# Kernel optimization log

Measured on AMD Instinct MI355X. Metric: run time of the kernel, lower is better.

## Reference

```python
import jax, jax.numpy as jnp
import numpy as np

NUM_NODES = 39   # nodes per graph (hardcoded in module)
K = 10           # kNN neighbors (hardcoded)
HID = 256
NUM_CLASSES = 2
B = 512          # number of graphs
EPS = 1e-5


def _edge_conv(xg, W, b):
    """DynamicEdgeConv with max aggregation.
    xg: [B, N, F]. Builds kNN graph per-graph (Euclidean), edge feature
    [x_i, x_j - x_i], MLP(ReLU), max over neighbors. Self is its own
    nearest neighbor (matches torch_cluster.knn with x==y).
    """
    bsz, n, f = xg.shape
    sq = jnp.sum(xg * xg, axis=-1)                      # [B, N]
    d = sq[:, :, None] + sq[:, None, :] - 2.0 * jnp.einsum('bnf,bmf->bnm', xg, xg)
    _, idx = jax.lax.top_k(-d, K)                       # [B, N, K] smallest distances
    xj = xg[jnp.arange(bsz)[:, None, None], idx]        # [B, N, K, F]
    xi = xg[:, :, None, :]                              # [B, N, 1, F]
    e = jnp.concatenate([jnp.broadcast_to(xi, xj.shape), xj - xi], axis=-1)  # [B,N,K,2F]
    h = jax.nn.relu(jnp.einsum('bnkc,ch->bnkh', e, W) + b)
    return jnp.max(h, axis=2)                           # [B, N, H]


def _bn(h, gamma, beta):
    # BatchNorm1d over all nodes (training-mode batch stats, biased var)
    mean = jnp.mean(h, axis=(0, 1), keepdims=True)
    var = jnp.var(h, axis=(0, 1), keepdims=True)
    return (h - mean) * jax.lax.rsqrt(var + EPS) * gamma + beta


def setup_inputs() -> dict:
    key = jax.random.key(0)
    ks = jax.random.split(key, 12)
    f_in = NUM_NODES
    x = jax.random.normal(ks[0], (B * NUM_NODES, f_in), dtype=jnp.float32)
    batch = jnp.repeat(jnp.arange(B, dtype=jnp.int32), NUM_NODES)
    def lin(k, fin, fout):
        s = 1.0 / np.sqrt(fin)
        k1, k2 = jax.random.split(k)
        W = jax.random.uniform(k1, (fin, fout), jnp.float32, -s, s)
        b = jax.random.uniform(k2, (fout,), jnp.float32, -s, s)
        return W, b
    W1, b1 = lin(ks[1], 2 * f_in, HID)
    W2, b2 = lin(ks[2], 2 * HID, HID)
    W3, b3 = lin(ks[3], 2 * HID, HID)
    Wl, bl = lin(ks[4], HID, NUM_CLASSES)
    g1 = jnp.ones((HID,), jnp.float32); be1 = jnp.zeros((HID,), jnp.float32)
    g2 = jnp.ones((HID,), jnp.float32); be2 = jnp.zeros((HID,), jnp.float32)
    g3 = jnp.ones((HID,), jnp.float32); be3 = jnp.zeros((HID,), jnp.float32)
    return dict(x=x, batch=batch, W1=W1, b1=b1, W2=W2, b2=b2, W3=W3, b3=b3,
                g1=g1, be1=be1, g2=g2, be2=be2, g3=g3, be3=be3, Wl=Wl, bl=bl)


def reference(x, batch, W1, b1, W2, b2, W3, b3, g1, be1, g2, be2, g3, be3, Wl, bl):
    # Graphs are contiguous with fixed NUM_NODES nodes each (batch == repeat(arange(B))),
    # so reshape implements per-graph kNN and global_mean_pool exactly.
    bsz = x.shape[0] // NUM_NODES
    xg = x.reshape(bsz, NUM_NODES, -1)
    h = _edge_conv(xg, W1, b1)
    h = jax.nn.relu(_bn(h, g1, be1))
    h = _edge_conv(h, W2, b2)
    h = jax.nn.relu(_bn(h, g2, be2))
    h = _edge_conv(h, W3, b3)
    h = _bn(h, g3, be3)
    pooled = jnp.mean(h, axis=1)                        # global_mean_pool -> [B, H]
    logits = pooled @ Wl + bl
    return jax.nn.softmax(logits, axis=1)
```

## Files before the change

### kernel.cpp

```cpp
#include <hip/hip_runtime.h>
#include <hip/hip_bf16.h>
#include <stdint.h>

#define NG 512
#define NN 39
#define FIN0 39
#define HID 256
#define KNN 10
#define NROWS (NG * NN)
#define BNEPS 1e-5f

typedef __hip_bfloat16 bf16;
typedef __attribute__((ext_vector_type(8))) short s16x8;
typedef __attribute__((ext_vector_type(4))) float f32x4;

__device__ __forceinline__ void split_bf16(float v, bf16& hi, bf16& lo) {
  hi = __float2bfloat16(v);
  lo = __float2bfloat16(v - __bfloat162float(hi));
}

__device__ __forceinline__ void ld_b128(s16x8& d, const bf16* base, unsigned voff) {
  asm volatile("global_load_dwordx4 %0, %1, %2" : "=v"(d) : "v"(voff), "s"(base));
}
__device__ __forceinline__ void ld_f32x4(f32x4& d, const float* base, unsigned voff) {
  asm volatile("global_load_dwordx4 %0, %1, %2" : "=v"(d) : "v"(voff), "s"(base));
}
#define WAITV4 do { asm volatile("s_waitcnt vmcnt(4)"); __builtin_amdgcn_sched_barrier(0); } while (0)
#define WAITV0 do { asm volatile("s_waitcnt vmcnt(0)"); __builtin_amdgcn_sched_barrier(0); } while (0)

__device__ __forceinline__ float wfold(const float* __restrict__ W, int F, int c, int k) {
  if (k >= F) return 0.f;
  return (c < HID) ? (W[k * HID + c] - W[(F + k) * HID + c])
                   : W[(F + k) * HID + (c - HID)];
}

__global__ void k_prepw(const float* __restrict__ W1, const float* __restrict__ W2,
                        const float* __restrict__ W3,
                        bf16* __restrict__ W1Th, bf16* __restrict__ W1Tl,
                        bf16* __restrict__ W2Th, bf16* __restrict__ W2Tl,
                        bf16* __restrict__ W3Th, bf16* __restrict__ W3Tl) {
  int d = (blockIdx.x * 256 + threadIdx.x) * 4;
  const float* W; bf16 *Th, *Tl; int nks, F;
  if (d < 512 * 64) { W = W1; Th = W1Th; Tl = W1Tl; nks = 2; F = FIN0; }
  else {
    d -= 512 * 64;
    if (d < 512 * 256) { W = W2; Th = W2Th; Tl = W2Tl; nks = 8; F = HID; }
    else {
      d -= 512 * 256;
      if (d < 512 * 256) { W = W3; Th = W3Th; Tl = W3Tl; nks = 8; F = HID; }
      else return;
    }
  }
  const int frag = d >> 9, wi = d & 511, li = wi >> 3, e0 = wi & 7;
  const int fr = li & 15, fq = li >> 4;
  const int ks = frag % nks, cb = frag / nks;
  const int c = (cb >> 2) * 64 + 4 * fr + (cb & 3);
  const int k0 = ks * 32 + fq * 8 + e0;
  union U { bf16 b[4]; uint64_t u; } h, l;
#pragma unroll
  for (int t = 0; t < 4; t++) split_bf16(wfold(W, F, c, k0 + t), h.b[t], l.b[t]);
  *(uint64_t*)(Th + d) = h.u;
  *(uint64_t*)(Tl + d) = l.u;
}

#define VSTR 260
#define RSTR 260
template <int K, bool FIRST>
__global__ __launch_bounds__(512, 4) void k_fused(const float* __restrict__ fin,
                                                  const float* __restrict__ st,
                                                  const bf16* __restrict__ BTh,
                                                  const bf16* __restrict__ BTl,
                                                  const float* __restrict__ bias,
                                                  float* __restrict__ h_out,
                                                  float* __restrict__ part) {
  constexpr int XBYTES = 48 * K * 2 * 2;
  constexpr int ALIAS = (NN * VSTR + 8 * RSTR) * 4;
  constexpr int SBASE = (XBYTES > ALIAS) ? XBYTES : ((ALIAS + 15) & ~15);
  __shared__ __align__(16) char smem[SBASE + 6240 + 160 + 1568];
  bf16* Xh = (bf16*)smem;
  bf16* Xl = Xh + 48 * K;
  float* vsh = (float*)smem;
  float* red = (float*)(smem + NN * VSTR * 4);
  float* dmat = (float*)(smem + SBASE);
  float* sqv  = (float*)(smem + SBASE + 6240);
  int*   idxs = (int*)(smem + SBASE + 6240 + 160);

  const int b = blockIdx.x, tid = threadIdx.x;
  const int wv = tid >> 6, ln = tid & 63;
  const int fr = ln & 15, fq = ln >> 4;
  const size_t base = (size_t)b * NN;
  constexpr int NKS = K / 32;

  if (FIRST) {
    if (tid < 48 * 8) {
      const int row = tid >> 3, g = tid & 7;
      union { bf16 b8[8]; s16x8 v; } ph, pl;
      if (row < NN) {
#pragma unroll
        for (int j = 0; j < 8; j++) {
          const int k = g * 8 + j;
          const float x = (k < FIN0) ? fin[(base + row) * FIN0 + k] : 0.f;
          split_bf16(x, ph.b8[j], pl.b8[j]);
        }
      } else {
#pragma unroll
        for (int j = 0; j < 8; j++) { ph.b8[j] = __float2bfloat16(0.f); pl.b8[j] = ph.b8[j]; }
      }
      const int ad = row * K + ((g ^ (row & 7)) << 3);
      *(s16x8*)&Xh[ad] = ph.v;
      *(s16x8*)&Xl[ad] = pl.v;
    }
  } else {
    const int r0 = tid >> 5, g = tid & 31;
    const unsigned o0 = (unsigned)((((base + r0) * HID) + g * 8) * 4);
    const unsigned rstep = (unsigned)(16 * HID * 4);
    f32x4 a0, a1, b0, b1, c0v, c1v;
    ld_f32x4(a0, fin, o0);             ld_f32x4(a1, fin, o0 + 16);
    ld_f32x4(b0, fin, o0 + rstep);     ld_f32x4(b1, fin, o0 + rstep + 16);
    ld_f32x4(c0v, fin, o0 + 2 * rstep); ld_f32x4(c1v, fin, o0 + 2 * rstep + 16);
    const f32x4 sc0 = *(const f32x4*)&st[g * 8];
    const f32x4 sc1 = *(const f32x4*)&st[g * 8 + 4];
    const f32x4 sh0 = *(const f32x4*)&st[HID + g * 8];
    const f32x4 sh1 = *(const f32x4*)&st[HID + g * 8 + 4];
    WAITV0;
    auto proc = [&](int row, const f32x4& lo4, const f32x4& hi4) {
      union { bf16 b8[8]; s16x8 v; } ph, pl;
#pragma unroll
      for (int j = 0; j < 4; j++) {
        const float v = fmaxf(lo4[j] * sc0[j] + sh0[j], 0.f);
        split_bf16(v, ph.b8[j], pl.b8[j]);
      }
#pragma unroll
      for (int j = 0; j < 4; j++) {
        const float v = fmaxf(hi4[j] * sc1[j] + sh1[j], 0.f);
        split_bf16(v, ph.b8[4 + j], pl.b8[4 + j]);
      }
      const int ad = row * K + ((g ^ (row & 7)) << 3);
      *(s16x8*)&Xh[ad] = ph.v;
      *(s16x8*)&Xl[ad] = pl.v;
    };
    proc(r0, a0, a1);
    proc(r0 + 16, b0, b1);
    const int r2 = r0 + 32;
    if (r2 < NN) proc(r2, c0v, c1v);
    else {
      union { bf16 b8[8]; s16x8 v; } z;
#pragma unroll
      for (int j = 0; j < 8; j++) z.b8[j] = __float2bfloat16(0.f);
      const int ad = r2 * K + ((g ^ (r2 & 7)) << 3);
      *(s16x8*)&Xh[ad] = z.v;
      *(s16x8*)&Xl[ad] = z.v;
    }
  }

  unsigned fb[4];
#pragma unroll
  for (int n = 0; n < 4; n++)
    fb[n] = ((unsigned)((wv * 4 + n) * NKS) << 10) + (unsigned)(ln * 16);
  s16x8 bufH[4], bufL[4];
#pragma unroll
  for (int n = 0; n < 4; n++) ld_b128(bufH[n], BTh, fb[n]);
  __syncthreads();

  for (int p = wv; p < 9; p += 8) {
    const int mi = p / 3, ni = p % 3;
    f32x4 acg = (f32x4){0.f, 0.f, 0.f, 0.f};
    const int ar = mi * 16 + fr, br = ni * 16 + fr;
#pragma unroll
    for (int ks = 0; ks < NKS; ks++) {
      const int ga = ((ks * 4 + fq) ^ (ar & 7)) << 3;
      const int gb = ((ks * 4 + fq) ^ (br & 7)) << 3;
      const s16x8 avh = *(const s16x8*)&Xh[ar * K + ga];
      const s16x8 avl = *(const s16x8*)&Xl[ar * K + ga];
      const s16x8 bvh = *(const s16x8*)&Xh[br * K + gb];
      const s16x8 bvl = *(const s16x8*)&Xl[br * K + gb];
      acg = __builtin_amdgcn_mfma_f32_16x16x32_bf16(avh, bvh, acg, 0, 0, 0);
      acg = __builtin_amdgcn_mfma_f32_16x16x32_bf16(avh, bvl, acg, 0, 0, 0);
      acg = __builtin_amdgcn_mfma_f32_16x16x32_bf16(avl, bvh, acg, 0, 0, 0);
    }
    const int oc = ni * 16 + fr;
    if (oc < NN) {
#pragma unroll
      for (int r = 0; r < 4; r++) {
        const int orow = mi * 16 + fq * 4 + r;
        if (orow < NN) dmat[orow * 40 + oc] = acg[r];
      }
    }
  }
  __syncthreads();

  if (tid < NN) sqv[tid] = dmat[tid * 40 + tid];
  __syncthreads();
  for (int t = tid; t < NN * NN; t += 512) {
    const int i = t / NN, j = t - i * NN;
    dmat[i * 40 + j] = sqv[i] + sqv[j] - 2.f * dmat[i * 40 + j];
  }
  __syncthreads();

  const int grp = tid >> 2, l4 = tid & 3;
  if (grp < NN) {
    float dv[10];
#pragma unroll
    for (int s = 0; s < 10; s++) {
      const int j = l4 + s * 4;
      dv[s] = (j < NN) ? dmat[grp * 40 + j] : 3.4e38f;
    }
    unsigned taken = 0;
    for (int k = 0; k < KNN; k++) {
      float bv = 3.4e38f;
      int bi = 1 << 30;
#pragma unroll
      for (int s = 0; s < 10; s++) {
        const float v = ((taken >> s) & 1u) ? 3.4e38f : dv[s];
        const int j = l4 + s * 4;
        if (v < bv || (v == bv && j < bi)) { bv = v; bi = j; }
      }
#pragma unroll
      for (int m = 1; m < 4; m <<= 1) {
        const float ov = __shfl_xor(bv, m, 64);
        const int oi = __shfl_xor(bi, m, 64);
        if (ov < bv || (ov == bv && oi < bi)) { bv = ov; bi = oi; }
      }
      if ((bi & 3) == l4) taken |= 1u << (bi >> 2);
      if (l4 == 0) idxs[grp * 10 + k] = bi;
    }
  }

  f32x4 acc[3][4];
#pragma unroll
  for (int m = 0; m < 3; m++)
#pragma unroll
    for (int n = 0; n < 4; n++) acc[m][n] = (f32x4){0.f, 0.f, 0.f, 0.f};

#pragma unroll
  for (int ks = 0; ks < NKS; ks++) {
#pragma unroll
    for (int n = 0; n < 4; n++) ld_b128(bufL[n], BTl, fb[n] + (unsigned)ks * 1024);
    s16x8 ah0, ah1, ah2, al0, al1, al2;
    {
      const int r0w = fr, r1w = 16 + fr, r2w = 32 + fr;
      const int g0 = ((ks * 4 + fq) ^ (r0w & 7)) << 3;
      const int g1 = ((ks * 4 + fq) ^ (r1w & 7)) << 3;
      const int g2 = ((ks * 4 + fq) ^ (r2w & 7)) << 3;
      ah0 = *(const s16x8*)&Xh[r0w * K + g0]; al0 = *(const s16x8*)&Xl[r0w * K + g0];
      ah1 = *(const s16x8*)&Xh[r1w * K + g1]; al1 = *(const s16x8*)&Xl[r1w * K + g1];
      ah2 = *(const s16x8*)&Xh[r2w * K + g2]; al2 = *(const s16x8*)&Xl[r2w * K + g2];
    }
    WAITV4;
#pragma unroll
    for (int n = 0; n < 4; n++) {
      acc[0][n] = __builtin_amdgcn_mfma_f32_16x16x32_bf16(ah0, bufH[n], acc[0][n], 0, 0, 0);
      acc[0][n] = __builtin_amdgcn_mfma_f32_16x16x32_bf16(al0, bufH[n], acc[0][n], 0, 0, 0);
      acc[1][n] = __builtin_amdgcn_mfma_f32_16x16x32_bf16(ah1, bufH[n], acc[1][n], 0, 0, 0);
      acc[1][n] = __builtin_amdgcn_mfma_f32_16x16x32_bf16(al1, bufH[n], acc[1][n], 0, 0, 0);
      acc[2][n] = __builtin_amdgcn_mfma_f32_16x16x32_bf16(ah2, bufH[n], acc[2][n], 0, 0, 0);
      acc[2][n] = __builtin_amdgcn_mfma_f32_16x16x32_bf16(al2, bufH[n], acc[2][n], 0, 0, 0);
    }
    if (ks + 1 < NKS) {
#pragma unroll
      for (int n = 0; n < 4; n++) ld_b128(bufH[n], BTh, fb[n] + (unsigned)(ks + 1) * 1024);
      WAITV4;
    } else {
      WAITV0;
    }
#pragma unroll
    for (int n = 0; n < 4; n++) {
      acc[0][n] = __builtin_amdgcn_mfma_f32_16x16x32_bf16(ah0, bufL[n], acc[0][n], 0, 0, 0);
      acc[1][n] = __builtin_amdgcn_mfma_f32_16x16x32_bf16(ah1, bufL[n], acc[1][n], 0, 0, 0);
      acc[2][n] = __builtin_amdgcn_mfma_f32_16x16x32_bf16(ah2, bufL[n], acc[2][n], 0, 0, 0);
    }
  }
  __syncthreads();

  if (wv >= 4) {
    const int c0 = (wv - 4) * 64 + fr * 4;
#pragma unroll
    for (int m = 0; m < 3; m++)
#pragma unroll
      for (int r = 0; r < 4; r++) {
        const int row = m * 16 + fq * 4 + r;
        if (row < NN) {
          const f32x4 v4 = (f32x4){acc[m][0][r], acc[m][1][r], acc[m][2][r], acc[m][3][r]};
          *(f32x4*)&vsh[row * VSTR + c0] = v4;
        }
      }
  } else {
    const int c0 = wv * 64 + fr * 4;
    const f32x4 bv = *(const f32x4*)&bias[c0];
#pragma unroll
    for (int n = 0; n < 4; n++)
#pragma unroll
      for (int m = 0; m < 3; m++)
#pragma unroll
        for (int r = 0; r < 4; r++) acc[m][n][r] += bv[n];
  }
  __syncthreads();

  if (wv < 4) {
    const int c0 = wv * 64 + fr * 4;
    f32x4 s1 = (f32x4){0.f, 0.f, 0.f, 0.f}, s2 = (f32x4){0.f, 0.f, 0.f, 0.f};
#pragma unroll
    for (int m = 0; m < 3; m++)
#pragma unroll
      for (int r = 0; r < 4; r++) {
        const int row = m * 16 + fq * 4 + r;
        if (row < NN) {
          int nb[10];
#pragma unroll
          for (int k = 0; k < KNN; k++) nb[k] = idxs[row * 10 + k];
          f32x4 vm = (f32x4){-3.4e38f, -3.4e38f, -3.4e38f, -3.4e38f};
#pragma unroll
          for (int k = 0; k < KNN; k++) {
            const f32x4 t4 = *(const f32x4*)&vsh[nb[k] * VSTR + c0];
            vm[0] = fmaxf(vm[0], t4[0]); vm[1] = fmaxf(vm[1], t4[1]);
            vm[2] = fmaxf(vm[2], t4[2]); vm[3] = fmaxf(vm[3], t4[3]);
          }
          f32x4 h4;
#pragma unroll
          for (int j = 0; j < 4; j++) h4[j] = fmaxf(acc[m][j][r] + vm[j], 0.f);
          *(f32x4*)&h_out[(size_t)(base + row) * HID + c0] = h4;
#pragma unroll
          for (int j = 0; j < 4; j++) { s1[j] += h4[j]; s2[j] += h4[j] * h4[j]; }
        }
      }
    *(f32x4*)&red[fq * RSTR + c0] = s1;
    *(f32x4*)&red[(4 + fq) * RSTR + c0] = s2;
  }
  __syncthreads();
  if (tid < HID) {
    part[(size_t)b * 512 + tid] =
        red[0 * RSTR + tid] + red[1 * RSTR + tid] + red[2 * RSTR + tid] + red[3 * RSTR + tid];
    part[(size_t)b * 512 + HID + tid] =
        red[4 * RSTR + tid] + red[5 * RSTR + tid] + red[6 * RSTR + tid] + red[7 * RSTR + tid];
  }
}

__global__ __launch_bounds__(256) void k_stats(const float* __restrict__ part,
                                               const float* __restrict__ gam,
                                               const float* __restrict__ bet,
                                               float* __restrict__ st) {
  __shared__ float rs[4], rq[4];
  const int c = blockIdx.x, tid = threadIdx.x;
  float s = part[(size_t)tid * 512 + c] + part[(size_t)(tid + 256) * 512 + c];
  float q = part[(size_t)tid * 512 + HID + c] + part[(size_t)(tid + 256) * 512 + HID + c];
#pragma unroll
  for (int m = 32; m >= 1; m >>= 1) { s += __shfl_down(s, m, 64); q += __shfl_down(q, m, 64); }
  if ((tid & 63) == 0) { rs[tid >> 6] = s; rq[tid >> 6] = q; }
  __syncthreads();
  if (tid == 0) {
    s = rs[0] + rs[1] + rs[2] + rs[3];
    q = rq[0] + rq[1] + rq[2] + rq[3];
    const float mean = s * (1.f / NROWS);
    const float var = q * (1.f / NROWS) - mean * mean;
    const float sc = gam[c] * rsqrtf(var + BNEPS);
    st[c] = sc;
    st[HID + c] = bet[c] - mean * sc;
  }
}

__global__ __launch_bounds__(256) void k_final(const float* __restrict__ h3,
                                               const float* __restrict__ st,
                                               const float* __restrict__ Wl,
                                               const float* __restrict__ bl,
                                               float* __restrict__ out) {
  __shared__ float r0[HID], r1[HID];
  const int b = blockIdx.x, c = threadIdx.x;
  float s = 0.f;
#pragma unroll 13
  for (int n = 0; n < NN; n++) s += h3[((size_t)b * NN + n) * HID + c];
  const float pooled = (s * (1.f / NN)) * st[c] + st[HID + c];
  r0[c] = pooled * Wl[c * 2 + 0];
  r1[c] = pooled * Wl[c * 2 + 1];
  __syncthreads();
  for (int stp = 128; stp > 0; stp >>= 1) {
    if (c < stp) { r0[c] += r0[c + stp]; r1[c] += r1[c + stp]; }
    __syncthreads();
  }
  if (c == 0) {
    const float l0 = r0[0] + bl[0], l1 = r1[0] + bl[1];
    const float mx = fmaxf(l0, l1);
    const float e0 = expf(l0 - mx), e1 = expf(l1 - mx);
    const float inv = 1.f / (e0 + e1);
    out[b * 2 + 0] = e0 * inv;
    out[b * 2 + 1] = e1 * inv;
  }
}

extern "C" void kernel_launch(void* const* d_in, const int* in_sizes, int n_in,
                              void* d_out, int out_size, void* d_ws, size_t ws_size,
                              hipStream_t stream) {
  const float* x   = (const float*)d_in[0];
  const float* W1  = (const float*)d_in[2];
  const float* b1  = (const float*)d_in[3];
  const float* W2  = (const float*)d_in[4];
  const float* b2  = (const float*)d_in[5];
  const float* W3  = (const float*)d_in[6];
  const float* b3  = (const float*)d_in[7];
  const float* g1  = (const float*)d_in[8];
  const float* be1 = (const float*)d_in[9];
  const float* g2  = (const float*)d_in[10];
  const float* be2 = (const float*)d_in[11];
  const float* g3  = (const float*)d_in[12];
  const float* be3 = (const float*)d_in[13];
  const float* Wl  = (const float*)d_in[14];
  const float* bl  = (const float*)d_in[15];

  char* ws = (char*)d_ws;
  size_t off = 0;
  auto alloc = [&](size_t bytes) {
    size_t o = off;
    off += (bytes + 255) & ~(size_t)255;
    return o;
  };
  bf16* W1Th = (bf16*)(ws + alloc(512 * 64 * 2));
  bf16* W1Tl = (bf16*)(ws + alloc(512 * 64 * 2));
  bf16* W2Th = (bf16*)(ws + alloc(512 * 256 * 2));
  bf16* W2Tl = (bf16*)(ws + alloc(512 * 256 * 2));
  bf16* W3Th = (bf16*)(ws + alloc(512 * 256 * 2));
  bf16* W3Tl = (bf16*)(ws + alloc(512 * 256 * 2));
  float* hA  = (float*)(ws + alloc((size_t)NROWS * HID * 4));
  float* hB  = (float*)(ws + alloc((size_t)NROWS * HID * 4));
  float* part = (float*)(ws + alloc((size_t)NG * 512 * 4));
  float* st1 = (float*)(ws + alloc(512 * 4));
  float* st2 = (float*)(ws + alloc(512 * 4));
  float* st3 = (float*)(ws + alloc(512 * 4));
  if (off > ws_size) return;

  k_prepw<<<288, 256, 0, stream>>>(W1, W2, W3, W1Th, W1Tl, W2Th, W2Tl, W3Th, W3Tl);

  k_fused<64, true><<<NG, 512, 0, stream>>>(x, nullptr, W1Th, W1Tl, b1, hA, part);
  k_stats<<<HID, 256, 0, stream>>>(part, g1, be1, st1);

  k_fused<256, false><<<NG, 512, 0, stream>>>(hA, st1, W2Th, W2Tl, b2, hB, part);
  k_stats<<<HID, 256, 0, stream>>>(part, g2, be2, st2);

  k_fused<256, false><<<NG, 512, 0, stream>>>(hB, st2, W3Th, W3Tl, b3, hA, part);
  k_stats<<<HID, 256, 0, stream>>>(part, g3, be3, st3);

  k_final<<<NG, 256, 0, stream>>>(hA, st3, Wl, bl, (float*)d_out);
}
```

Measured before the change: 99.56 us.

## Skip layer-3 activation write, pool from partial sums, transpose partials layout

The third edge-conv no longer writes its 20k x 256 activation tensor; the final kernel instead reads the per-graph column sums already stored in the partials buffer, since BN is affine and mean pooling commutes with it. The partials buffer is transposed to channel-major so the stats and final kernels read it contiguously. The kNN distance fixup pass and its two barriers are folded into the selection loads, and weight prep uses a shared-memory transpose for coalesced reads. This removes a large global write and read plus some block-wide syncs, while relying on the per-graph sums being exact enough for pooling.

```diff
diff --git a/kernel.cpp b/kernel.cpp
--- a/kernel.cpp
+++ b/kernel.cpp
@@ -28,44 +28,52 @@
 #define WAITV4 do { asm volatile("s_waitcnt vmcnt(4)"); __builtin_amdgcn_sched_barrier(0); } while (0)
 #define WAITV0 do { asm volatile("s_waitcnt vmcnt(0)"); __builtin_amdgcn_sched_barrier(0); } while (0)
 
-__device__ __forceinline__ float wfold(const float* __restrict__ W, int F, int c, int k) {
-  if (k >= F) return 0.f;
-  return (c < HID) ? (W[k * HID + c] - W[(F + k) * HID + c])
-                   : W[(F + k) * HID + (c - HID)];
-}
-
-__global__ void k_prepw(const float* __restrict__ W1, const float* __restrict__ W2,
-                        const float* __restrict__ W3,
-                        bf16* __restrict__ W1Th, bf16* __restrict__ W1Tl,
-                        bf16* __restrict__ W2Th, bf16* __restrict__ W2Tl,
-                        bf16* __restrict__ W3Th, bf16* __restrict__ W3Tl) {
-  int d = (blockIdx.x * 256 + threadIdx.x) * 4;
-  const float* W; bf16 *Th, *Tl; int nks, F;
-  if (d < 512 * 64) { W = W1; Th = W1Th; Tl = W1Tl; nks = 2; F = FIN0; }
-  else {
-    d -= 512 * 64;
-    if (d < 512 * 256) { W = W2; Th = W2Th; Tl = W2Tl; nks = 8; F = HID; }
-    else {
-      d -= 512 * 256;
-      if (d < 512 * 256) { W = W3; Th = W3Th; Tl = W3Tl; nks = 8; F = HID; }
-      else return;
-    }
-  }
-  const int frag = d >> 9, wi = d & 511, li = wi >> 3, e0 = wi & 7;
-  const int fr = li & 15, fq = li >> 4;
-  const int ks = frag % nks, cb = frag / nks;
-  const int c = (cb >> 2) * 64 + 4 * fr + (cb & 3);
-  const int k0 = ks * 32 + fq * 8 + e0;
-  union U { bf16 b[4]; uint64_t u; } h, l;
-#pragma unroll
-  for (int t = 0; t < 4; t++) split_bf16(wfold(W, F, c, k0 + t), h.b[t], l.b[t]);
-  *(uint64_t*)(Th + d) = h.u;
-  *(uint64_t*)(Tl + d) = l.u;
+__global__ __launch_bounds__(256) void k_prepw(const float* __restrict__ W1,
+                                               const float* __restrict__ W2,
+                                               const float* __restrict__ W3,
+                                               bf16* __restrict__ W1Th, bf16* __restrict__ W1Tl,
+                                               bf16* __restrict__ W2Th, bf16* __restrict__ W2Tl,
+                                               bf16* __restrict__ W3Th, bf16* __restrict__ W3Tl) {
+  __shared__ float tile[32][65];
+  const int blk = blockIdx.x, tid = threadIdx.x;
+  const float* W; bf16 *Th, *Tl; int NKS_, F, colblock, ks;
+  if (blk < 16)      { W = W1; Th = W1Th; Tl = W1Tl; NKS_ = 2; F = FIN0; colblock = blk >> 1;        ks = blk & 1; }
+  else if (blk < 80) { W = W2; Th = W2Th; Tl = W2Tl; NKS_ = 8; F = HID;  colblock = (blk - 16) >> 3; ks = (blk - 16) & 7; }
+  else               { W = W3; Th = W3Th; Tl = W3Tl; NKS_ = 8; F = HID;  colblock = (blk - 80) >> 3; ks = (blk - 80) & 7; }
+
+  const int kl = tid >> 3, cseg = (tid & 7) * 8;
+  const int k = ks * 32 + kl;
+  const int cg = colblock * 64 + cseg;
+  float v[8];
+  if (k < F) {
+    if (colblock < 4) {
+#pragma unroll
+      for (int j = 0; j < 8; j++) v[j] = W[k * HID + cg + j] - W[(F + k) * HID + cg + j];
+    } else {
+#pragma unroll
+      for (int j = 0; j < 8; j++) v[j] = W[(F + k) * HID + (cg - 256) + j];
+    }
+  } else {
+#pragma unroll
+    for (int j = 0; j < 8; j++) v[j] = 0.f;
+  }
+#pragma unroll
+  for (int j = 0; j < 8; j++) tile[kl][cseg + j] = v[j];
+  __syncthreads();
+
+  const int q = tid >> 6, li = tid & 63, fr = li & 15, fq = li >> 4;
+  const int cl = 4 * fr + q;
+  union { bf16 b8[8]; s16x8 s; } hh, ll;
+#pragma unroll
+  for (int e = 0; e < 8; e++) split_bf16(tile[fq * 8 + e][cl], hh.b8[e], ll.b8[e]);
+  const size_t frag = (size_t)((colblock * 4 + q) * NKS_ + ks);
+  *(s16x8*)(Th + frag * 512 + li * 8) = hh.s;
+  *(s16x8*)(Tl + frag * 512 + li * 8) = ll.s;
 }
 
 #define VSTR 260
 #define RSTR 260
-template <int K, bool FIRST>
+template <int K, bool FIRST, bool WH>
 __global__ __launch_bounds__(512, 4) void k_fused(const float* __restrict__ fin,
                                                   const float* __restrict__ st,
                                                   const bf16* __restrict__ BTh,
@@ -82,7 +90,6 @@
   float* vsh = (float*)smem;
   float* red = (float*)(smem + NN * VSTR * 4);
   float* dmat = (float*)(smem + SBASE);
-  float* sqv  = (float*)(smem + SBASE + 6240);
   int*   idxs = (int*)(smem + SBASE + 6240 + 160);
 
   const int b = blockIdx.x, tid = threadIdx.x;
@@ -99,8 +106,8 @@
 #pragma unroll
         for (int j = 0; j < 8; j++) {
           const int k = g * 8 + j;
-          const float x = (k < FIN0) ? fin[(base + row) * FIN0 + k] : 0.f;
-          split_bf16(x, ph.b8[j], pl.b8[j]);
+          const float xv = (k < FIN0) ? fin[(base + row) * FIN0 + k] : 0.f;
+          split_bf16(xv, ph.b8[j], pl.b8[j]);
         }
       } else {
 #pragma unroll
@@ -115,8 +122,8 @@
     const unsigned o0 = (unsigned)((((base + r0) * HID) + g * 8) * 4);
     const unsigned rstep = (unsigned)(16 * HID * 4);
     f32x4 a0, a1, b0, b1, c0v, c1v;
-    ld_f32x4(a0, fin, o0);             ld_f32x4(a1, fin, o0 + 16);
-    ld_f32x4(b0, fin, o0 + rstep);     ld_f32x4(b1, fin, o0 + rstep + 16);
+    ld_f32x4(a0, fin, o0);              ld_f32x4(a1, fin, o0 + 16);
+    ld_f32x4(b0, fin, o0 + rstep);      ld_f32x4(b1, fin, o0 + rstep + 16);
     ld_f32x4(c0v, fin, o0 + 2 * rstep); ld_f32x4(c1v, fin, o0 + 2 * rstep + 16);
     const f32x4 sc0 = *(const f32x4*)&st[g * 8];
     const f32x4 sc1 = *(const f32x4*)&st[g * 8 + 4];
@@ -189,21 +196,14 @@
   }
   __syncthreads();
 
-  if (tid < NN) sqv[tid] = dmat[tid * 40 + tid];
-  __syncthreads();
-  for (int t = tid; t < NN * NN; t += 512) {
-    const int i = t / NN, j = t - i * NN;
-    dmat[i * 40 + j] = sqv[i] + sqv[j] - 2.f * dmat[i * 40 + j];
-  }
-  __syncthreads();
-
   const int grp = tid >> 2, l4 = tid & 3;
   if (grp < NN) {
+    const float sqg = dmat[grp * 40 + grp];
     float dv[10];
 #pragma unroll
     for (int s = 0; s < 10; s++) {
       const int j = l4 + s * 4;
-      dv[s] = (j < NN) ? dmat[grp * 40 + j] : 3.4e38f;
+      dv[s] = (j < NN) ? (sqg + dmat[j * 40 + j] - 2.f * dmat[grp * 40 + j]) : 3.4e38f;
     }
     unsigned taken = 0;
     for (int k = 0; k < KNN; k++) {
@@ -318,7 +318,7 @@
           f32x4 h4;
 #pragma unroll
           for (int j = 0; j < 4; j++) h4[j] = fmaxf(acc[m][j][r] + vm[j], 0.f);
-          *(f32x4*)&h_out[(size_t)(base + row) * HID + c0] = h4;
+          if (WH) *(f32x4*)&h_out[(size_t)(base + row) * HID + c0] = h4;
 #pragma unroll
           for (int j = 0; j < 4; j++) { s1[j] += h4[j]; s2[j] += h4[j] * h4[j]; }
         }
@@ -328,9 +328,9 @@
   }
   __syncthreads();
   if (tid < HID) {
-    part[(size_t)b * 512 + tid] =
+    part[(size_t)tid * NG + b] =
         red[0 * RSTR + tid] + red[1 * RSTR + tid] + red[2 * RSTR + tid] + red[3 * RSTR + tid];
-    part[(size_t)b * 512 + HID + tid] =
+    part[(size_t)(HID + tid) * NG + b] =
         red[4 * RSTR + tid] + red[5 * RSTR + tid] + red[6 * RSTR + tid] + red[7 * RSTR + tid];
   }
 }
@@ -341,8 +341,8 @@
                                                float* __restrict__ st) {
   __shared__ float rs[4], rq[4];
   const int c = blockIdx.x, tid = threadIdx.x;
-  float s = part[(size_t)tid * 512 + c] + part[(size_t)(tid + 256) * 512 + c];
-  float q = part[(size_t)tid * 512 + HID + c] + part[(size_t)(tid + 256) * 512 + HID + c];
+  float s = part[(size_t)c * NG + tid] + part[(size_t)c * NG + tid + 256];
+  float q = part[(size_t)(HID + c) * NG + tid] + part[(size_t)(HID + c) * NG + tid + 256];
 #pragma unroll
   for (int m = 32; m >= 1; m >>= 1) { s += __shfl_down(s, m, 64); q += __shfl_down(q, m, 64); }
   if ((tid & 63) == 0) { rs[tid >> 6] = s; rq[tid >> 6] = q; }
@@ -358,16 +358,14 @@
   }
 }
 
-__global__ __launch_bounds__(256) void k_final(const float* __restrict__ h3,
+__global__ __launch_bounds__(256) void k_final(const float* __restrict__ part,
                                                const float* __restrict__ st,
                                                const float* __restrict__ Wl,
                                                const float* __restrict__ bl,
                                                float* __restrict__ out) {
   __shared__ float r0[HID], r1[HID];
   const int b = blockIdx.x, c = threadIdx.x;
-  float s = 0.f;
-#pragma unroll 13
-  for (int n = 0; n < NN; n++) s += h3[((size_t)b * NN + n) * HID + c];
+  const float s = part[(size_t)c * NG + b];
   const float pooled = (s * (1.f / NN)) * st[c] + st[HID + c];
   r0[c] = pooled * Wl[c * 2 + 0];
   r1[c] = pooled * Wl[c * 2 + 1];
@@ -420,22 +418,22 @@
   bf16* W3Tl = (bf16*)(ws + alloc(512 * 256 * 2));
   float* hA  = (float*)(ws + alloc((size_t)NROWS * HID * 4));
   float* hB  = (float*)(ws + alloc((size_t)NROWS * HID * 4));
-  float* part = (float*)(ws + alloc((size_t)NG * 512 * 4));
+  float* part = (float*)(ws + alloc((size_t)512 * NG * 4));
   float* st1 = (float*)(ws + alloc(512 * 4));
   float* st2 = (float*)(ws + alloc(512 * 4));
   float* st3 = (float*)(ws + alloc(512 * 4));
   if (off > ws_size) return;
 
-  k_prepw<<<288, 256, 0, stream>>>(W1, W2, W3, W1Th, W1Tl, W2Th, W2Tl, W3Th, W3Tl);
-
-  k_fused<64, true><<<NG, 512, 0, stream>>>(x, nullptr, W1Th, W1Tl, b1, hA, part);
+  k_prepw<<<144, 256, 0, stream>>>(W1, W2, W3, W1Th, W1Tl, W2Th, W2Tl, W3Th, W3Tl);
+
+  k_fused<64, true, true><<<NG, 512, 0, stream>>>(x, nullptr, W1Th, W1Tl, b1, hA, part);
   k_stats<<<HID, 256, 0, stream>>>(part, g1, be1, st1);
 
-  k_fused<256, false><<<NG, 512, 0, stream>>>(hA, st1, W2Th, W2Tl, b2, hB, part);
+  k_fused<256, false, true><<<NG, 512, 0, stream>>>(hA, st1, W2Th, W2Tl, b2, hB, part);
   k_stats<<<HID, 256, 0, stream>>>(part, g2, be2, st2);
 
-  k_fused<256, false><<<NG, 512, 0, stream>>>(hB, st2, W3Th, W3Tl, b3, hA, part);
+  k_fused<256, false, false><<<NG, 512, 0, stream>>>(hB, st2, W3Th, W3Tl, b3, nullptr, part);
   k_stats<<<HID, 256, 0, stream>>>(part, g3, be3, st3);
 
-  k_final<<<NG, 256, 0, stream>>>(hA, st3, Wl, bl, (float*)d_out);
-}
+  k_final<<<NG, 256, 0, stream>>>(part, st3, Wl, bl, (float*)d_out);
+}
```

New measurement: 143.7 us. +44.3%, slower.
